# Optimization experiments

Measured on AMD Instinct MI355X. Metric: run time of the kernel, lower is better.

## Reference

```python
import jax, jax.numpy as jnp
import numpy as np

D_MODEL = 1024
N_HEADS = 16
MIXTURE_FACTOR = 4
LATENT = D_MODEL // MIXTURE_FACTOR  # 256
D_K = D_MODEL // N_HEADS            # 64
B, L = 2, 2048


def setup_inputs() -> dict:
    key = jax.random.key(0)
    ks = jax.random.split(key, 13)
    s_in = 1.0 / np.sqrt(D_MODEL)
    s_lat = 1.0 / np.sqrt(LATENT)
    return {
        "queries": jax.random.normal(ks[0], (B, L, 1, D_MODEL), jnp.float32),
        "keys": jax.random.normal(ks[1], (B, L, 1, D_MODEL), jnp.float32),
        "values": jax.random.normal(ks[2], (B, L, 1, D_MODEL), jnp.float32),
        "Wq": jax.random.normal(ks[3], (D_MODEL, D_MODEL), jnp.float32) * s_in,
        "bq": jnp.zeros((D_MODEL,), jnp.float32),
        "Wd": jax.random.normal(ks[4], (D_MODEL, LATENT), jnp.float32) * s_in,
        "bd": jnp.zeros((LATENT,), jnp.float32),
        "Wk": jax.random.normal(ks[5], (LATENT, D_MODEL), jnp.float32) * s_lat,
        "bk": jnp.zeros((D_MODEL,), jnp.float32),
        "Wv": jax.random.normal(ks[6], (LATENT, D_MODEL), jnp.float32) * s_lat,
        "bv": jnp.zeros((D_MODEL,), jnp.float32),
        "Wo": jax.random.normal(ks[7], (D_MODEL, D_MODEL), jnp.float32) * s_in,
        "bo": jnp.zeros((D_MODEL,), jnp.float32),
    }


def reference(queries, keys, values, Wq, bq, Wd, bd, Wk, bk, Wv, bv, Wo, bo):
    b, l, h_in, e = queries.shape  # h_in == 1, e == d_model
    s = keys.shape[1]
    scale = D_K ** -0.5

    q_flat = queries.reshape(b, l, e)
    Q = (q_flat @ Wq + bq).reshape(b, l, N_HEADS, D_K)

    kv_input = keys.reshape(b, s, e)
    latent = kv_input @ Wd + bd                      # [b, s, latent]
    K = (latent @ Wk + bk).reshape(b, s, N_HEADS, D_K)
    V = (latent @ Wv + bv).reshape(b, s, N_HEADS, D_K)

    scores = jnp.einsum('blhe,bshe->bhls', Q, K) * scale  # [b, h, l, s]
    causal = jnp.triu(jnp.ones((l, s), dtype=bool), k=1)
    scores = jnp.where(causal, -jnp.inf, scores)
    A = jax.nn.softmax(scores, axis=-1)

    out = jnp.einsum('bhls,bshd->blhd', A, V).reshape(b, l, N_HEADS * D_K)
    return out @ Wo + bo
```

## Files before the change

### kernel.cpp

```cpp
#include <hip/hip_runtime.h>
#include <stdint.h>


#define DM 1024
#define NH 16
#define DK 64
#define LL 2048

typedef float  f32x4  __attribute__((ext_vector_type(4)));
typedef __bf16 bf16x8 __attribute__((ext_vector_type(8)));
typedef short  s16x8  __attribute__((ext_vector_type(8)));

__device__ __forceinline__ unsigned short f2bf(float f) {
    union { float f; unsigned int u; } v; v.f = f;
    return (unsigned short)((v.u + 0x7fffu + ((v.u >> 16) & 1u)) >> 16);
}
__device__ __forceinline__ unsigned int pack2(float a, float b) {
    return (unsigned int)f2bf(a) | ((unsigned int)f2bf(b) << 16);
}
__device__ __forceinline__ unsigned int packt(float a, float b) {
    union { float f; unsigned int u; } x, y; x.f = a; y.f = b;
    return (x.u >> 16) | (y.u & 0xffff0000u);
}
__device__ __forceinline__ bf16x8 ld8(const unsigned short* p) {
    s16x8 s = *(const s16x8*)p;
    return __builtin_bit_cast(bf16x8, s);
}
__device__ __forceinline__ void gl16(const void* g, void* l) {
    __builtin_amdgcn_global_load_lds((__attribute__((address_space(1))) void*)(g),
                                     (__attribute__((address_space(3))) void*)(l),
                                     16, 0, 0);
}

__global__ __launch_bounds__(256)
void prep_k(const float* __restrict__ Wq, const float* __restrict__ Wd,
            const float* __restrict__ Wk, const float* __restrict__ Wv,
            const float* __restrict__ Wo, const float* __restrict__ queries,
            const float* __restrict__ keys,
            unsigned short* __restrict__ WqT, unsigned short* __restrict__ WdT,
            unsigned short* __restrict__ WkvT, unsigned short* __restrict__ WoT,
            unsigned short* __restrict__ Qb, unsigned short* __restrict__ Kb) {
    int bid = blockIdx.x;
    const int t = threadIdx.x;

    const float* W; unsigned short* WT; int TK, TN;
    if (bid < 1024)      { W = Wq; WT = WqT;  TK = 1024; TN = 1024; }
    else if (bid < 1280) { bid -= 1024; W = Wd; WT = WdT; TK = 1024; TN = 256; }
    else if (bid < 1536) { bid -= 1280; W = Wk; WT = WkvT; TK = 256; TN = 1024; }
    else if (bid < 1792) { bid -= 1536; W = Wv; WT = WkvT + (size_t)1024 * 256; TK = 256; TN = 1024; }
    else if (bid < 2816) { bid -= 1792; W = Wo; WT = WoT;  TK = 1024; TN = 1024; }
    else {
        bid -= 2816;
        const float* src; unsigned short* dst;
        if (bid < 1024) { src = queries; dst = Qb; }
        else            { bid -= 1024; src = keys; dst = Kb; }
        const size_t base = (size_t)bid * 4096;
#pragma unroll
        for (int i = 0; i < 4; ++i) {
            float4 f = *(const float4*)(src + base + (size_t)(i * 256 + t) * 4);
            uint2 u = { pack2(f.x, f.y), pack2(f.z, f.w) };
            *(uint2*)(dst + base + (size_t)(i * 256 + t) * 4) = u;
        }
        return;
    }
    __shared__ float tile[32][33];
    const int tx = t & 31, ty = t >> 5;
    const int bx = bid % (TK / 32), by = bid / (TK / 32);
    const int k0 = bx * 32, n0 = by * 32;
#pragma unroll
    for (int i = 0; i < 4; ++i)
        tile[ty + 8 * i][tx] = W[(size_t)(k0 + ty + 8 * i) * TN + n0 + tx];
    __syncthreads();
#pragma unroll
    for (int i = 0; i < 4; ++i)
        WT[(size_t)(n0 + ty + 8 * i) * TK + k0 + tx] = f2bf(tile[tx][ty + 8 * i]);
}

__device__ __forceinline__ void stage6(const unsigned short* gA, const unsigned short* gB,
                                       int kk, int K,
                                       unsigned short* lA, unsigned short* lB) {
#pragma unroll
    for (int s = 0; s < 4; ++s) gl16(gA + kk + (size_t)s * 8 * K, lA + s * 512);
#pragma unroll
    for (int s = 0; s < 2; ++s) gl16(gB + kk + (size_t)s * 8 * K, lB + s * 512);
}

__device__ __forceinline__ void mfma16(const unsigned short* As, const unsigned short* Bs,
                                       const int aoff[4][2], const int boff[2][2],
                                       f32x4 acc[4][2]) {
#pragma unroll
    for (int ks = 0; ks < 2; ++ks) {
        bf16x8 a[4], b[2];
#pragma unroll
        for (int i = 0; i < 4; ++i) a[i] = ld8(As + aoff[i][ks]);
#pragma unroll
        for (int j = 0; j < 2; ++j) b[j] = ld8(Bs + boff[j][ks]);
#pragma unroll
        for (int i = 0; i < 4; ++i)
#pragma unroll
            for (int j = 0; j < 2; ++j)
                acc[i][j] = __builtin_amdgcn_mfma_f32_16x16x32_bf16(a[i], b[j], acc[i][j], 0, 0, 0);
    }
}

template<int MODE>
__global__ __launch_bounds__(256)
void gemm_k(const unsigned short* __restrict__ Ap, const unsigned short* __restrict__ Bt,
            const float* __restrict__ bias, void* __restrict__ Cp,
            const unsigned short* __restrict__ Ap2, const unsigned short* __restrict__ Bt2,
            const float* __restrict__ bias2, void* __restrict__ Cp2,
            int K) {
    __shared__ unsigned short Sh0[12288];
    __shared__ unsigned short Sh1[12288];

    int bid = blockIdx.x;
    const unsigned short* A;
    const unsigned short* B;
    const float* bs;
    bool second = false;
    int m0, n0;
    if (MODE == 0 && bid >= 512) {
        bid -= 512; A = Ap2; B = Bt2; bs = bias2; second = true;
        const int xcd = bid & 7, s = bid >> 3;
        n0 = (s & 3) * 64; m0 = (xcd * 4 + (s >> 2)) * 128;
    } else {
        A = Ap; B = Bt; bs = bias;
        const int xcd = bid & 7, s = bid >> 3;
        if (MODE == 2) { n0 = (s & 31) * 64; m0 = (xcd * 4 + (s >> 5)) * 128; }
        else           { n0 = (s & 15) * 64; m0 = (xcd * 4 + (s >> 4)) * 128; }
    }

    const int t = threadIdx.x, lane = t & 63, wv = t >> 6;
    const int quad = lane >> 4, l15 = lane & 15;

    const int lr8 = lane >> 3;
    const int g8 = (lane & 7) ^ (lr8 & 7);
    const unsigned short* gA = A + (size_t)(m0 + wv * 32 + lr8) * K + g8 * 8;
    const unsigned short* gB = B + (size_t)(n0 + wv * 16 + lr8) * K + g8 * 8;
    unsigned short* lA0 = Sh0 + wv * 2048;
    unsigned short* lB0 = Sh0 + 8192 + wv * 1024;
    unsigned short* lA1 = Sh1 + wv * 2048;
    unsigned short* lB1 = Sh1 + 8192 + wv * 1024;

    int aoff[4][2], boff[2][2];
#pragma unroll
    for (int i = 0; i < 4; ++i) {
        const int ra = (wv >> 1) * 64 + i * 16 + l15;
#pragma unroll
        for (int ks = 0; ks < 2; ++ks)
            aoff[i][ks] = ra * 64 + (((ks * 4 + quad) ^ (ra & 7)) << 3);
    }
#pragma unroll
    for (int j = 0; j < 2; ++j) {
        const int rb = (wv & 1) * 32 + j * 16 + l15;
#pragma unroll
        for (int ks = 0; ks < 2; ++ks)
            boff[j][ks] = rb * 64 + (((ks * 4 + quad) ^ (rb & 7)) << 3);
    }

    f32x4 acc[4][2] = {};
    const int niter = K >> 6;

    stage6(gA, gB, 0, K, lA0, lB0);
    __syncthreads();
    for (int it = 0; it < niter; it += 2) {
        const int kk = it << 6;
        if (it + 1 < niter) stage6(gA, gB, kk + 64, K, lA1, lB1);
        mfma16(Sh0, Sh0 + 8192, aoff, boff, acc);
        __syncthreads();
        if (it + 1 < niter) {
            if (it + 2 < niter) stage6(gA, gB, kk + 128, K, lA0, lB0);
            mfma16(Sh1, Sh1 + 8192, aoff, boff, acc);
            __syncthreads();
        }
    }

    const bool isV = (MODE == 2) && (n0 >= 1024);
    if (!isV) {
#pragma unroll
        for (int j = 0; j < 2; ++j) {
            const int col = n0 + (wv & 1) * 32 + j * 16 + l15;
            const float bvv = bs[col];
#pragma unroll
            for (int i = 0; i < 4; ++i) {
                const int rowb = m0 + (wv >> 1) * 64 + i * 16 + quad * 4;
#pragma unroll
                for (int r = 0; r < 4; ++r) {
                    const float v = acc[i][j][r] + bvv;
                    const int row = rowb + r;
                    if (MODE == 1)
                        ((float*)Cp)[(size_t)row * 1024 + col] = v;
                    else if (second)
                        ((unsigned short*)Cp2)[(size_t)row * 256 + col] = f2bf(v);
                    else
                        ((unsigned short*)Cp)[(size_t)row * 1024 + col] = f2bf(v);
                }
            }
        }
    } else {
        unsigned short* Ld = Sh0;
#pragma unroll
        for (int j = 0; j < 2; ++j) {
            const int dloc = (wv & 1) * 32 + j * 16 + l15;
            const float bvv = bias2[(n0 - 1024) + dloc];
#pragma unroll
            for (int i = 0; i < 4; ++i) {
                const int tokb = (wv >> 1) * 64 + i * 16 + quad * 4;
#pragma unroll
                for (int r = 0; r < 4; ++r)
                    Ld[dloc * 136 + tokb + r] = f2bf(acc[i][j][r] + bvv);
            }
        }
        __syncthreads();
        const int dloc = t >> 2;
        const int tk0 = (t & 3) * 32;
        const int bb = m0 >> 11;
        unsigned short* dst = (unsigned short*)Cp2 +
            ((size_t)bb * 1024 + (n0 - 1024) + dloc) * LL + (m0 & (LL - 1)) + tk0;
        const unsigned short* srcp = Ld + dloc * 136 + tk0;
#pragma unroll
        for (int c = 0; c < 4; ++c)
            *(uint4*)(dst + c * 8) = *(const uint4*)(srcp + c * 8);
    }
}

__global__ __launch_bounds__(512, 4)
void attn8_k(const unsigned short* __restrict__ Qp,
             const unsigned short* __restrict__ Kp,
             const unsigned short* __restrict__ VpT,
             unsigned short* __restrict__ Op) {
    __shared__ unsigned short Ks[2][2][4096];
    __shared__ unsigned short Vs[2][4096];
    __shared__ unsigned short Ps[8][1152];
    float* CB = (float*)&Ks[0][0][0];

    const int t = threadIdx.x, lane = t & 63, wv = t >> 6;
    const int grp = wv >> 2, w4 = wv & 3;
    const int quad = lane >> 4, l15 = lane & 15;

    const int bid = blockIdx.x;
    const int xcd = bid & 7, s = bid >> 3;
    const int pair = s & 15;
    const int combo = xcd * 4 + (s >> 4);
    const int h = combo & 15, b = combo >> 4;

    const int srow = w4 * 16 + (lane >> 3);
    const int g8 = (lane & 7) ^ ((lane >> 3) & 7);
    const int sw = l15 & 7;
    unsigned short* PsW = Ps[wv];

    const unsigned short* Kbase = Kp + (size_t)(b * LL + srow) * DM + h * DK + g8 * 8;
    const unsigned short* Vbase = VpT + ((size_t)(b * NH + h) * DK + srow) * LL + g8 * 8;
    unsigned short* lV = &Vs[grp][w4 * 1024];

    for (int tsel = 0; tsel < 2; ++tsel) {
        const int tile = tsel ? (31 - pair) : pair;
        const int q0 = tile * 64;
        const int rowq = q0 + w4 * 16 + l15;

        if (tsel) __syncthreads();

        const unsigned short* qp = Qp + (size_t)(b * LL + rowq) * DM + h * DK;
        const bf16x8 aq0 = ld8(qp + quad * 8);
        const bf16x8 aq1 = ld8(qp + 32 + quad * 8);

        f32x4 acc[4] = {};
        float lsum = 0.f;

        if (grp <= tile) {
            const unsigned short* kg = Kbase + (size_t)(grp * 64) * DM;
            unsigned short* lK = &Ks[grp][0][w4 * 1024];
            gl16(kg, lK); gl16(kg + (size_t)8 * DM, lK + 512);
        }

        const int nit = tile / 2 + 1;
        for (int it = 0; it < nit; ++it) {
            const int c = 2 * it + grp;
            const int cur = it & 1;
            const bool active = (c <= tile);
            const int kt = c * 64;

            if (active) {
                const unsigned short* vg = Vbase + kt;
                gl16(vg, lV); gl16(vg + (size_t)8 * LL, lV + 512);
                const int c2 = (c + 2 <= tile) ? (c + 2) : tile;
                const unsigned short* kg = Kbase + (size_t)(c2 * 64) * DM;
                unsigned short* lK = &Ks[grp][cur ^ 1][w4 * 1024];
                gl16(kg, lK); gl16(kg + (size_t)8 * DM, lK + 512);
            }
            asm volatile("s_waitcnt vmcnt(4)" ::: "memory");
            __builtin_amdgcn_s_barrier();
            __builtin_amdgcn_sched_barrier(0);

            if (active) {
                const unsigned short* Kc = Ks[grp][cur];
                const bool diag = (c == tile);
#pragma unroll
                for (int sub = 0; sub < 4; ++sub) {
                    const int base2 = (sub * 16 + l15) * 64;
                    const bf16x8 k0 = ld8(Kc + base2 + ((quad ^ sw) << 3));
                    const bf16x8 k1 = ld8(Kc + base2 + (((4 + quad) ^ sw) << 3));
                    f32x4 ss = {};
                    ss = __builtin_amdgcn_mfma_f32_16x16x32_bf16(k0, aq0, ss, 0, 0, 0);
                    ss = __builtin_amdgcn_mfma_f32_16x16x32_bf16(k1, aq1, ss, 0, 0, 0);
                    float e[4];
                    if (diag) {
                        const int kb4 = kt + sub * 16 + quad * 4;
#pragma unroll
                        for (int r = 0; r < 4; ++r) {
                            const float x = exp2f(fmaf(ss[r], 0.18033688011112042f, -16.0f));
                            e[r] = (kb4 + r > rowq) ? 0.f : x;
                        }
                    } else {
#pragma unroll
                        for (int r = 0; r < 4; ++r)
                            e[r] = exp2f(fmaf(ss[r], 0.18033688011112042f, -16.0f));
                    }
                    lsum += (e[0] + e[1]) + (e[2] + e[3]);
                    uint2 w2;
                    w2.x = packt(e[0], e[1]);
                    w2.y = packt(e[2], e[3]);
                    *(uint2*)(PsW + l15 * 72 + sub * 16 + quad * 4) = w2;
                }
            }
            asm volatile("s_waitcnt vmcnt(2)" ::: "memory");
            __builtin_amdgcn_s_barrier();
            __builtin_amdgcn_sched_barrier(0);

            if (active) {
#pragma unroll
                for (int ks = 0; ks < 2; ++ks) {
                    const bf16x8 ap = ld8(PsW + l15 * 72 + ks * 32 + quad * 8);
#pragma unroll
                    for (int sub = 0; sub < 4; ++sub) {
                        const bf16x8 bv = ld8(&Vs[grp][(sub * 16 + l15) * 64 +
                                                       (((ks * 4 + quad) ^ sw) << 3)]);
                        acc[sub] = __builtin_amdgcn_mfma_f32_16x16x32_bf16(ap, bv, acc[sub], 0, 0, 0);
                    }
                }
            }
            __builtin_amdgcn_s_barrier();
            __builtin_amdgcn_sched_barrier(0);
        }

        __syncthreads();
        const int base = (w4 * 64 + lane) * 20;
        if (grp == 1) {
#pragma unroll
            for (int sub = 0; sub < 4; ++sub)
#pragma unroll
                for (int r = 0; r < 4; ++r) CB[base + sub * 4 + r] = acc[sub][r];
            CB[base + 16] = lsum;
        }
        __syncthreads();
        if (grp == 0) {
#pragma unroll
            for (int sub = 0; sub < 4; ++sub)
#pragma unroll
                for (int r = 0; r < 4; ++r) acc[sub][r] += CB[base + sub * 4 + r];
            lsum += CB[base + 16];
            lsum += __shfl_xor(lsum, 16, 64);
            lsum += __shfl_xor(lsum, 32, 64);
            const float inv = __builtin_amdgcn_rcpf(lsum);
            float invr[4];
#pragma unroll
            for (int r = 0; r < 4; ++r) invr[r] = __shfl(inv, quad * 4 + r, 64);
#pragma unroll
            for (int sub = 0; sub < 4; ++sub)
#pragma unroll
                for (int r = 0; r < 4; ++r)
                    Op[(size_t)(b * LL + q0 + w4 * 16 + quad * 4 + r) * DM + h * DK + sub * 16 + l15] =
                        f2bf(acc[sub][r] * invr[r]);
        }
    }
}

extern "C" void kernel_launch(void* const* d_in, const int* in_sizes, int n_in,
                              void* d_out, int out_size, void* d_ws, size_t ws_size,
                              hipStream_t stream) {
    const float* queries = (const float*)d_in[0];
    const float* keys    = (const float*)d_in[1];
    const float* Wq = (const float*)d_in[3];  const float* bq = (const float*)d_in[4];
    const float* Wd = (const float*)d_in[5];  const float* bd = (const float*)d_in[6];
    const float* Wk = (const float*)d_in[7];  const float* bk = (const float*)d_in[8];
    const float* Wv = (const float*)d_in[9];  const float* bv = (const float*)d_in[10];
    const float* Wo = (const float*)d_in[11]; const float* bo = (const float*)d_in[12];

    char* ws = (char*)d_ws;
    const size_t MB = 1048576;
    unsigned short* Qp   = (unsigned short*)(ws);
    unsigned short* Kb   = (unsigned short*)(ws + 8 * MB);
    unsigned short* Kp   = (unsigned short*)(ws + 8 * MB);
    unsigned short* Qb   = (unsigned short*)(ws + 16 * MB);
    unsigned short* VpT  = (unsigned short*)(ws + 16 * MB);
    unsigned short* WqT  = (unsigned short*)(ws + 24 * MB);
    unsigned short* Lat  = (unsigned short*)(ws + 26 * MB);
    unsigned short* WdT  = (unsigned short*)(ws + 28 * MB);
    unsigned short* WkvT = (unsigned short*)(ws + 28 * MB + 524288);
    unsigned short* Attn = (unsigned short*)(ws + 24 * MB);
    unsigned short* WoT  = (unsigned short*)(ws + 32 * MB);

    prep_k<<<4864, 256, 0, stream>>>(Wq, Wd, Wk, Wv, Wo, queries, keys,
                                     WqT, WdT, WkvT, WoT, Qb, Kb);
    gemm_k<0><<<640, 256, 0, stream>>>(Qb, WqT, bq, Qp, Kb, WdT, bd, Lat, 1024);
    gemm_k<2><<<1024, 256, 0, stream>>>(Lat, WkvT, bk, Kp, nullptr, nullptr, bv, VpT, 256);
    attn8_k<<<512, 512, 0, stream>>>(Qp, Kp, VpT, Attn);
    gemm_k<1><<<512, 256, 0, stream>>>(Attn, WoT, bo, d_out, nullptr, nullptr, nullptr, nullptr, 1024);
}
```

Measured before the change: 202.2 us.

## Share K/V tile loads between paired query tiles in one causal attention sweep

The attention kernel now processes its two query tiles (pair and 31-pair) in a single pass over key blocks instead of two sequential passes. Each K/V tile loaded into LDS is used for both tiles when the smaller tile is still active, which removes the duplicate global loads for the short tile. It also wraps the MFMA sections in s_setprio raises. The cost is doubled accumulator registers and a longer serial inner phase per iteration, where the A-tile QK and PV run back to back through the same P buffer, which could hurt occupancy or latency hiding.

```diff
diff --git a/kernel.cpp b/kernel.cpp
--- a/kernel.cpp
+++ b/kernel.cpp
@@ -224,8 +224,57 @@
     }
 }
 
+__device__ __forceinline__ void qk_sm(const unsigned short* Kc,
+        const bf16x8 aq0, const bf16x8 aq1, int rowq, int kt, bool diag,
+        int l15, int quad, int sw, unsigned short* PsW, float& lsum) {
+#pragma unroll
+    for (int sub = 0; sub < 4; ++sub) {
+        const int base2 = (sub * 16 + l15) * 64;
+        const bf16x8 k0 = ld8(Kc + base2 + ((quad ^ sw) << 3));
+        const bf16x8 k1 = ld8(Kc + base2 + (((4 + quad) ^ sw) << 3));
+        f32x4 ss = {};
+        __builtin_amdgcn_s_setprio(1);
+        ss = __builtin_amdgcn_mfma_f32_16x16x32_bf16(k0, aq0, ss, 0, 0, 0);
+        ss = __builtin_amdgcn_mfma_f32_16x16x32_bf16(k1, aq1, ss, 0, 0, 0);
+        __builtin_amdgcn_s_setprio(0);
+        float e[4];
+        if (diag) {
+            const int kb4 = kt + sub * 16 + quad * 4;
+#pragma unroll
+            for (int r = 0; r < 4; ++r) {
+                const float x = exp2f(fmaf(ss[r], 0.18033688011112042f, -16.0f));
+                e[r] = (kb4 + r > rowq) ? 0.f : x;
+            }
+        } else {
+#pragma unroll
+            for (int r = 0; r < 4; ++r)
+                e[r] = exp2f(fmaf(ss[r], 0.18033688011112042f, -16.0f));
+        }
+        lsum += (e[0] + e[1]) + (e[2] + e[3]);
+        uint2 w2;
+        w2.x = packt(e[0], e[1]);
+        w2.y = packt(e[2], e[3]);
+        *(uint2*)(PsW + l15 * 72 + sub * 16 + quad * 4) = w2;
+    }
+}
+
+__device__ __forceinline__ void pv_acc(const unsigned short* PsW, const unsigned short* Vg,
+        int l15, int quad, int sw, f32x4 acc[4]) {
+#pragma unroll
+    for (int ks = 0; ks < 2; ++ks) {
+        const bf16x8 ap = ld8(PsW + l15 * 72 + ks * 32 + quad * 8);
+        __builtin_amdgcn_s_setprio(1);
+#pragma unroll
+        for (int sub = 0; sub < 4; ++sub) {
+            const bf16x8 bv = ld8(Vg + (sub * 16 + l15) * 64 + (((ks * 4 + quad) ^ sw) << 3));
+            acc[sub] = __builtin_amdgcn_mfma_f32_16x16x32_bf16(ap, bv, acc[sub], 0, 0, 0);
+        }
+        __builtin_amdgcn_s_setprio(0);
+    }
+}
+
 __global__ __launch_bounds__(512, 4)
-void attn8_k(const unsigned short* __restrict__ Qp,
+void attn9_k(const unsigned short* __restrict__ Qp,
              const unsigned short* __restrict__ Kp,
              const unsigned short* __restrict__ VpT,
              unsigned short* __restrict__ Op) {
@@ -244,6 +293,8 @@
     const int combo = xcd * 4 + (s >> 4);
     const int h = combo & 15, b = combo >> 4;
 
+    const int tA = pair, tB = 31 - pair;
+
     const int srow = w4 * 16 + (lane >> 3);
     const int g8 = (lane & 7) ^ ((lane >> 3) & 7);
     const int sw = l15 & 7;
@@ -253,125 +304,117 @@
     const unsigned short* Vbase = VpT + ((size_t)(b * NH + h) * DK + srow) * LL + g8 * 8;
     unsigned short* lV = &Vs[grp][w4 * 1024];
 
-    for (int tsel = 0; tsel < 2; ++tsel) {
-        const int tile = tsel ? (31 - pair) : pair;
-        const int q0 = tile * 64;
-        const int rowq = q0 + w4 * 16 + l15;
-
-        if (tsel) __syncthreads();
-
-        const unsigned short* qp = Qp + (size_t)(b * LL + rowq) * DM + h * DK;
-        const bf16x8 aq0 = ld8(qp + quad * 8);
-        const bf16x8 aq1 = ld8(qp + 32 + quad * 8);
-
-        f32x4 acc[4] = {};
-        float lsum = 0.f;
-
-        if (grp <= tile) {
-            const unsigned short* kg = Kbase + (size_t)(grp * 64) * DM;
-            unsigned short* lK = &Ks[grp][0][w4 * 1024];
+    const int rowqA = tA * 64 + w4 * 16 + l15;
+    const int rowqB = tB * 64 + w4 * 16 + l15;
+    const unsigned short* qpA = Qp + (size_t)(b * LL + rowqA) * DM + h * DK;
+    const unsigned short* qpB = Qp + (size_t)(b * LL + rowqB) * DM + h * DK;
+    const bf16x8 aqA0 = ld8(qpA + quad * 8), aqA1 = ld8(qpA + 32 + quad * 8);
+    const bf16x8 aqB0 = ld8(qpB + quad * 8), aqB1 = ld8(qpB + 32 + quad * 8);
+
+    f32x4 accA[4] = {}, accB[4] = {};
+    float lsumA = 0.f, lsumB = 0.f;
+
+    {
+        const unsigned short* kg = Kbase + (size_t)(grp * 64) * DM;
+        unsigned short* lK = &Ks[grp][0][w4 * 1024];
+        gl16(kg, lK); gl16(kg + (size_t)8 * DM, lK + 512);
+    }
+    const int lastc = tB - ((tB ^ grp) & 1);
+
+    const int nit = tB / 2 + 1;
+    for (int it = 0; it < nit; ++it) {
+        const int c = 2 * it + grp;
+        const int cur = it & 1;
+        const bool activeB = (c <= tB);
+        const bool activeA = (c <= tA);
+        const int kt = c * 64;
+
+        if (activeB) {
+            const unsigned short* vg = Vbase + kt;
+            gl16(vg, lV); gl16(vg + (size_t)8 * LL, lV + 512);
+            const int c2 = (c + 2 <= lastc) ? (c + 2) : lastc;
+            const unsigned short* kg = Kbase + (size_t)(c2 * 64) * DM;
+            unsigned short* lK = &Ks[grp][cur ^ 1][w4 * 1024];
             gl16(kg, lK); gl16(kg + (size_t)8 * DM, lK + 512);
         }
-
-        const int nit = tile / 2 + 1;
-        for (int it = 0; it < nit; ++it) {
-            const int c = 2 * it + grp;
-            const int cur = it & 1;
-            const bool active = (c <= tile);
-            const int kt = c * 64;
-
-            if (active) {
-                const unsigned short* vg = Vbase + kt;
-                gl16(vg, lV); gl16(vg + (size_t)8 * LL, lV + 512);
-                const int c2 = (c + 2 <= tile) ? (c + 2) : tile;
-                const unsigned short* kg = Kbase + (size_t)(c2 * 64) * DM;
-                unsigned short* lK = &Ks[grp][cur ^ 1][w4 * 1024];
-                gl16(kg, lK); gl16(kg + (size_t)8 * DM, lK + 512);
-            }
-            asm volatile("s_waitcnt vmcnt(4)" ::: "memory");
-            __builtin_amdgcn_s_barrier();
-            __builtin_amdgcn_sched_barrier(0);
-
-            if (active) {
-                const unsigned short* Kc = Ks[grp][cur];
-                const bool diag = (c == tile);
-#pragma unroll
-                for (int sub = 0; sub < 4; ++sub) {
-                    const int base2 = (sub * 16 + l15) * 64;
-                    const bf16x8 k0 = ld8(Kc + base2 + ((quad ^ sw) << 3));
-                    const bf16x8 k1 = ld8(Kc + base2 + (((4 + quad) ^ sw) << 3));
-                    f32x4 ss = {};
-                    ss = __builtin_amdgcn_mfma_f32_16x16x32_bf16(k0, aq0, ss, 0, 0, 0);
-                    ss = __builtin_amdgcn_mfma_f32_16x16x32_bf16(k1, aq1, ss, 0, 0, 0);
-                    float e[4];
-                    if (diag) {
-                        const int kb4 = kt + sub * 16 + quad * 4;
-#pragma unroll
-                        for (int r = 0; r < 4; ++r) {
-                            const float x = exp2f(fmaf(ss[r], 0.18033688011112042f, -16.0f));
-                            e[r] = (kb4 + r > rowq) ? 0.f : x;
-                        }
-                    } else {
-#pragma unroll
-                        for (int r = 0; r < 4; ++r)
-                            e[r] = exp2f(fmaf(ss[r], 0.18033688011112042f, -16.0f));
-                    }
-                    lsum += (e[0] + e[1]) + (e[2] + e[3]);
-                    uint2 w2;
-                    w2.x = packt(e[0], e[1]);
-                    w2.y = packt(e[2], e[3]);
-                    *(uint2*)(PsW + l15 * 72 + sub * 16 + quad * 4) = w2;
-                }
-            }
-            asm volatile("s_waitcnt vmcnt(2)" ::: "memory");
-            __builtin_amdgcn_s_barrier();
-            __builtin_amdgcn_sched_barrier(0);
-
-            if (active) {
-#pragma unroll
-                for (int ks = 0; ks < 2; ++ks) {
-                    const bf16x8 ap = ld8(PsW + l15 * 72 + ks * 32 + quad * 8);
-#pragma unroll
-                    for (int sub = 0; sub < 4; ++sub) {
-                        const bf16x8 bv = ld8(&Vs[grp][(sub * 16 + l15) * 64 +
-                                                       (((ks * 4 + quad) ^ sw) << 3)]);
-                        acc[sub] = __builtin_amdgcn_mfma_f32_16x16x32_bf16(ap, bv, acc[sub], 0, 0, 0);
-                    }
-                }
-            }
-            __builtin_amdgcn_s_barrier();
-            __builtin_amdgcn_sched_barrier(0);
-        }
-
-        __syncthreads();
-        const int base = (w4 * 64 + lane) * 20;
-        if (grp == 1) {
-#pragma unroll
-            for (int sub = 0; sub < 4; ++sub)
-#pragma unroll
-                for (int r = 0; r < 4; ++r) CB[base + sub * 4 + r] = acc[sub][r];
-            CB[base + 16] = lsum;
-        }
-        __syncthreads();
-        if (grp == 0) {
-#pragma unroll
-            for (int sub = 0; sub < 4; ++sub)
-#pragma unroll
-                for (int r = 0; r < 4; ++r) acc[sub][r] += CB[base + sub * 4 + r];
-            lsum += CB[base + 16];
-            lsum += __shfl_xor(lsum, 16, 64);
-            lsum += __shfl_xor(lsum, 32, 64);
-            const float inv = __builtin_amdgcn_rcpf(lsum);
-            float invr[4];
-#pragma unroll
-            for (int r = 0; r < 4; ++r) invr[r] = __shfl(inv, quad * 4 + r, 64);
-#pragma unroll
-            for (int sub = 0; sub < 4; ++sub)
-#pragma unroll
-                for (int r = 0; r < 4; ++r)
-                    Op[(size_t)(b * LL + q0 + w4 * 16 + quad * 4 + r) * DM + h * DK + sub * 16 + l15] =
-                        f2bf(acc[sub][r] * invr[r]);
-        }
+        asm volatile("s_waitcnt vmcnt(4)" ::: "memory");
+        __builtin_amdgcn_s_barrier();
+        __builtin_amdgcn_sched_barrier(0);
+
+        const unsigned short* Kc = Ks[grp][cur];
+        if (activeB)
+            qk_sm(Kc, aqB0, aqB1, rowqB, kt, c == tB, l15, quad, sw, PsW, lsumB);
+
+        asm volatile("s_waitcnt vmcnt(2)" ::: "memory");
+        __builtin_amdgcn_s_barrier();
+        __builtin_amdgcn_sched_barrier(0);
+
+        if (activeB)
+            pv_acc(PsW, &Vs[grp][0], l15, quad, sw, accB);
+        if (activeA) {
+            qk_sm(Kc, aqA0, aqA1, rowqA, kt, c == tA, l15, quad, sw, PsW, lsumA);
+            pv_acc(PsW, &Vs[grp][0], l15, quad, sw, accA);
+        }
+        __builtin_amdgcn_s_barrier();
+        __builtin_amdgcn_sched_barrier(0);
+    }
+
+    __syncthreads();
+    const int base = (w4 * 64 + lane) * 20;
+    if (grp == 1) {
+#pragma unroll
+        for (int sub = 0; sub < 4; ++sub)
+#pragma unroll
+            for (int r = 0; r < 4; ++r) CB[base + sub * 4 + r] = accA[sub][r];
+        CB[base + 16] = lsumA;
+    }
+    __syncthreads();
+    if (grp == 0) {
+#pragma unroll
+        for (int sub = 0; sub < 4; ++sub)
+#pragma unroll
+            for (int r = 0; r < 4; ++r) accA[sub][r] += CB[base + sub * 4 + r];
+        lsumA += CB[base + 16];
+        lsumA += __shfl_xor(lsumA, 16, 64);
+        lsumA += __shfl_xor(lsumA, 32, 64);
+        const float inv = __builtin_amdgcn_rcpf(lsumA);
+        float invr[4];
+#pragma unroll
+        for (int r = 0; r < 4; ++r) invr[r] = __shfl(inv, quad * 4 + r, 64);
+#pragma unroll
+        for (int sub = 0; sub < 4; ++sub)
+#pragma unroll
+            for (int r = 0; r < 4; ++r)
+                Op[(size_t)(b * LL + tA * 64 + w4 * 16 + quad * 4 + r) * DM + h * DK + sub * 16 + l15] =
+                    f2bf(accA[sub][r] * invr[r]);
+    }
+    __syncthreads();
+    if (grp == 1) {
+#pragma unroll
+        for (int sub = 0; sub < 4; ++sub)
+#pragma unroll
+            for (int r = 0; r < 4; ++r) CB[base + sub * 4 + r] = accB[sub][r];
+        CB[base + 16] = lsumB;
+    }
+    __syncthreads();
+    if (grp == 0) {
+#pragma unroll
+        for (int sub = 0; sub < 4; ++sub)
+#pragma unroll
+            for (int r = 0; r < 4; ++r) accB[sub][r] += CB[base + sub * 4 + r];
+        lsumB += CB[base + 16];
+        lsumB += __shfl_xor(lsumB, 16, 64);
+        lsumB += __shfl_xor(lsumB, 32, 64);
+        const float inv = __builtin_amdgcn_rcpf(lsumB);
+        float invr[4];
+#pragma unroll
+        for (int r = 0; r < 4; ++r) invr[r] = __shfl(inv, quad * 4 + r, 64);
+#pragma unroll
+        for (int sub = 0; sub < 4; ++sub)
+#pragma unroll
+            for (int r = 0; r < 4; ++r)
+                Op[(size_t)(b * LL + tB * 64 + w4 * 16 + quad * 4 + r) * DM + h * DK + sub * 16 + l15] =
+                    f2bf(accB[sub][r] * invr[r]);
     }
 }
 
@@ -404,6 +447,6 @@
                                      WqT, WdT, WkvT, WoT, Qb, Kb);
     gemm_k<0><<<640, 256, 0, stream>>>(Qb, WqT, bq, Qp, Kb, WdT, bd, Lat, 1024);
     gemm_k<2><<<1024, 256, 0, stream>>>(Lat, WkvT, bk, Kp, nullptr, nullptr, bv, VpT, 256);
-    attn8_k<<<512, 512, 0, stream>>>(Qp, Kp, VpT, Attn);
+    attn9_k<<<512, 512, 0, stream>>>(Qp, Kp, VpT, Attn);
     gemm_k<1><<<512, 256, 0, stream>>>(Attn, WoT, bo, d_out, nullptr, nullptr, nullptr, nullptr, 1024);
 }
```

Result: slower. 207.0 us (+2.3%).

## Replace split-KV paired-tile attention with one-tile-per-block 256-thread kernel

Applied to the files above, without the earlier changes.

The attention kernel previously had each 512-thread block process two query tiles (pair and 31-pair), splitting the KV range between two wave groups and merging their partial results through LDS. The new kernel launches 1024 blocks of 256 threads, each handling one query tile with a single-group double-buffered KV loop and no cross-group reduction. Tiles are ordered long-first within each XCD slot, relying on the hardware scheduler for causal load balancing. s_setprio is also added around the MFMA sections. This removes the merge and the idle-group iterations, but a single wave group per tile now serialises the KV loop and gives less intra-block parallelism per tile.

```diff
diff --git a/kernel.cpp b/kernel.cpp
--- a/kernel.cpp
+++ b/kernel.cpp
@@ -224,155 +224,135 @@
     }
 }
 
-__global__ __launch_bounds__(512, 4)
-void attn8_k(const unsigned short* __restrict__ Qp,
-             const unsigned short* __restrict__ Kp,
-             const unsigned short* __restrict__ VpT,
-             unsigned short* __restrict__ Op) {
-    __shared__ unsigned short Ks[2][2][4096];
-    __shared__ unsigned short Vs[2][4096];
-    __shared__ unsigned short Ps[8][1152];
-    float* CB = (float*)&Ks[0][0][0];
+__device__ __forceinline__ void qk_sm(const unsigned short* Kc,
+        const bf16x8 aq0, const bf16x8 aq1, int rowq, int kt, bool diag,
+        int l15, int quad, int sw, unsigned short* PsW, float& lsum) {
+#pragma unroll
+    for (int sub = 0; sub < 4; ++sub) {
+        const int base2 = (sub * 16 + l15) * 64;
+        const bf16x8 k0 = ld8(Kc + base2 + ((quad ^ sw) << 3));
+        const bf16x8 k1 = ld8(Kc + base2 + (((4 + quad) ^ sw) << 3));
+        f32x4 ss = {};
+        __builtin_amdgcn_s_setprio(1);
+        ss = __builtin_amdgcn_mfma_f32_16x16x32_bf16(k0, aq0, ss, 0, 0, 0);
+        ss = __builtin_amdgcn_mfma_f32_16x16x32_bf16(k1, aq1, ss, 0, 0, 0);
+        __builtin_amdgcn_s_setprio(0);
+        float e[4];
+        if (diag) {
+            const int kb4 = kt + sub * 16 + quad * 4;
+#pragma unroll
+            for (int r = 0; r < 4; ++r) {
+                const float x = exp2f(fmaf(ss[r], 0.18033688011112042f, -16.0f));
+                e[r] = (kb4 + r > rowq) ? 0.f : x;
+            }
+        } else {
+#pragma unroll
+            for (int r = 0; r < 4; ++r)
+                e[r] = exp2f(fmaf(ss[r], 0.18033688011112042f, -16.0f));
+        }
+        lsum += (e[0] + e[1]) + (e[2] + e[3]);
+        uint2 w2;
+        w2.x = packt(e[0], e[1]);
+        w2.y = packt(e[2], e[3]);
+        *(uint2*)(PsW + l15 * 72 + sub * 16 + quad * 4) = w2;
+    }
+}
+
+__device__ __forceinline__ void pv_acc(const unsigned short* PsW, const unsigned short* Vg,
+        int l15, int quad, int sw, f32x4 acc[4]) {
+#pragma unroll
+    for (int ks = 0; ks < 2; ++ks) {
+        const bf16x8 ap = ld8(PsW + l15 * 72 + ks * 32 + quad * 8);
+        __builtin_amdgcn_s_setprio(1);
+#pragma unroll
+        for (int sub = 0; sub < 4; ++sub) {
+            const bf16x8 bv = ld8(Vg + (sub * 16 + l15) * 64 + (((ks * 4 + quad) ^ sw) << 3));
+            acc[sub] = __builtin_amdgcn_mfma_f32_16x16x32_bf16(ap, bv, acc[sub], 0, 0, 0);
+        }
+        __builtin_amdgcn_s_setprio(0);
+    }
+}
+
+__global__ __launch_bounds__(256, 4)
+void attn10_k(const unsigned short* __restrict__ Qp,
+              const unsigned short* __restrict__ Kp,
+              const unsigned short* __restrict__ VpT,
+              unsigned short* __restrict__ Op) {
+    __shared__ unsigned short Ks[2][4096];
+    __shared__ unsigned short Vs[4096];
+    __shared__ unsigned short Ps[4][1152];
 
     const int t = threadIdx.x, lane = t & 63, wv = t >> 6;
-    const int grp = wv >> 2, w4 = wv & 3;
     const int quad = lane >> 4, l15 = lane & 15;
 
     const int bid = blockIdx.x;
     const int xcd = bid & 7, s = bid >> 3;
-    const int pair = s & 15;
-    const int combo = xcd * 4 + (s >> 4);
+    const int cu = s & 31, slot = s >> 5;
+    const int combo = xcd * 4 + slot;
+    const int tile = (slot & 1) ? cu : (31 - cu);
     const int h = combo & 15, b = combo >> 4;
-
-    const int srow = w4 * 16 + (lane >> 3);
+    const int q0 = tile * 64;
+
+    const int srow = wv * 16 + (lane >> 3);
     const int g8 = (lane & 7) ^ ((lane >> 3) & 7);
     const int sw = l15 & 7;
     unsigned short* PsW = Ps[wv];
 
     const unsigned short* Kbase = Kp + (size_t)(b * LL + srow) * DM + h * DK + g8 * 8;
     const unsigned short* Vbase = VpT + ((size_t)(b * NH + h) * DK + srow) * LL + g8 * 8;
-    unsigned short* lV = &Vs[grp][w4 * 1024];
-
-    for (int tsel = 0; tsel < 2; ++tsel) {
-        const int tile = tsel ? (31 - pair) : pair;
-        const int q0 = tile * 64;
-        const int rowq = q0 + w4 * 16 + l15;
-
-        if (tsel) __syncthreads();
-
-        const unsigned short* qp = Qp + (size_t)(b * LL + rowq) * DM + h * DK;
-        const bf16x8 aq0 = ld8(qp + quad * 8);
-        const bf16x8 aq1 = ld8(qp + 32 + quad * 8);
-
-        f32x4 acc[4] = {};
-        float lsum = 0.f;
-
-        if (grp <= tile) {
-            const unsigned short* kg = Kbase + (size_t)(grp * 64) * DM;
-            unsigned short* lK = &Ks[grp][0][w4 * 1024];
-            gl16(kg, lK); gl16(kg + (size_t)8 * DM, lK + 512);
-        }
-
-        const int nit = tile / 2 + 1;
-        for (int it = 0; it < nit; ++it) {
-            const int c = 2 * it + grp;
-            const int cur = it & 1;
-            const bool active = (c <= tile);
-            const int kt = c * 64;
-
-            if (active) {
-                const unsigned short* vg = Vbase + kt;
-                gl16(vg, lV); gl16(vg + (size_t)8 * LL, lV + 512);
-                const int c2 = (c + 2 <= tile) ? (c + 2) : tile;
-                const unsigned short* kg = Kbase + (size_t)(c2 * 64) * DM;
-                unsigned short* lK = &Ks[grp][cur ^ 1][w4 * 1024];
-                gl16(kg, lK); gl16(kg + (size_t)8 * DM, lK + 512);
-            }
-            asm volatile("s_waitcnt vmcnt(4)" ::: "memory");
-            __builtin_amdgcn_s_barrier();
-            __builtin_amdgcn_sched_barrier(0);
-
-            if (active) {
-                const unsigned short* Kc = Ks[grp][cur];
-                const bool diag = (c == tile);
-#pragma unroll
-                for (int sub = 0; sub < 4; ++sub) {
-                    const int base2 = (sub * 16 + l15) * 64;
-                    const bf16x8 k0 = ld8(Kc + base2 + ((quad ^ sw) << 3));
-                    const bf16x8 k1 = ld8(Kc + base2 + (((4 + quad) ^ sw) << 3));
-                    f32x4 ss = {};
-                    ss = __builtin_amdgcn_mfma_f32_16x16x32_bf16(k0, aq0, ss, 0, 0, 0);
-                    ss = __builtin_amdgcn_mfma_f32_16x16x32_bf16(k1, aq1, ss, 0, 0, 0);
-                    float e[4];
-                    if (diag) {
-                        const int kb4 = kt + sub * 16 + quad * 4;
-#pragma unroll
-                        for (int r = 0; r < 4; ++r) {
-                            const float x = exp2f(fmaf(ss[r], 0.18033688011112042f, -16.0f));
-                            e[r] = (kb4 + r > rowq) ? 0.f : x;
-                        }
-                    } else {
-#pragma unroll
-                        for (int r = 0; r < 4; ++r)
-                            e[r] = exp2f(fmaf(ss[r], 0.18033688011112042f, -16.0f));
-                    }
-                    lsum += (e[0] + e[1]) + (e[2] + e[3]);
-                    uint2 w2;
-                    w2.x = packt(e[0], e[1]);
-                    w2.y = packt(e[2], e[3]);
-                    *(uint2*)(PsW + l15 * 72 + sub * 16 + quad * 4) = w2;
-                }
-            }
-            asm volatile("s_waitcnt vmcnt(2)" ::: "memory");
-            __builtin_amdgcn_s_barrier();
-            __builtin_amdgcn_sched_barrier(0);
-
-            if (active) {
-#pragma unroll
-                for (int ks = 0; ks < 2; ++ks) {
-                    const bf16x8 ap = ld8(PsW + l15 * 72 + ks * 32 + quad * 8);
-#pragma unroll
-                    for (int sub = 0; sub < 4; ++sub) {
-                        const bf16x8 bv = ld8(&Vs[grp][(sub * 16 + l15) * 64 +
-                                                       (((ks * 4 + quad) ^ sw) << 3)]);
-                        acc[sub] = __builtin_amdgcn_mfma_f32_16x16x32_bf16(ap, bv, acc[sub], 0, 0, 0);
-                    }
-                }
-            }
-            __builtin_amdgcn_s_barrier();
-            __builtin_amdgcn_sched_barrier(0);
-        }
-
-        __syncthreads();
-        const int base = (w4 * 64 + lane) * 20;
-        if (grp == 1) {
-#pragma unroll
-            for (int sub = 0; sub < 4; ++sub)
-#pragma unroll
-                for (int r = 0; r < 4; ++r) CB[base + sub * 4 + r] = acc[sub][r];
-            CB[base + 16] = lsum;
-        }
-        __syncthreads();
-        if (grp == 0) {
-#pragma unroll
-            for (int sub = 0; sub < 4; ++sub)
-#pragma unroll
-                for (int r = 0; r < 4; ++r) acc[sub][r] += CB[base + sub * 4 + r];
-            lsum += CB[base + 16];
-            lsum += __shfl_xor(lsum, 16, 64);
-            lsum += __shfl_xor(lsum, 32, 64);
-            const float inv = __builtin_amdgcn_rcpf(lsum);
-            float invr[4];
-#pragma unroll
-            for (int r = 0; r < 4; ++r) invr[r] = __shfl(inv, quad * 4 + r, 64);
-#pragma unroll
-            for (int sub = 0; sub < 4; ++sub)
-#pragma unroll
-                for (int r = 0; r < 4; ++r)
-                    Op[(size_t)(b * LL + q0 + w4 * 16 + quad * 4 + r) * DM + h * DK + sub * 16 + l15] =
-                        f2bf(acc[sub][r] * invr[r]);
-        }
-    }
+    unsigned short* lV = Vs + wv * 1024;
+
+    const int rowq = q0 + wv * 16 + l15;
+    const unsigned short* qp = Qp + (size_t)(b * LL + rowq) * DM + h * DK;
+    const bf16x8 aq0 = ld8(qp + quad * 8);
+    const bf16x8 aq1 = ld8(qp + 32 + quad * 8);
+
+    f32x4 acc[4] = {};
+    float lsum = 0.f;
+
+    gl16(Kbase, Ks[0] + wv * 1024);
+    gl16(Kbase + (size_t)8 * DM, Ks[0] + wv * 1024 + 512);
+
+    for (int c = 0; c <= tile; ++c) {
+        const int cur = c & 1;
+        const int kt = c * 64;
+
+        const unsigned short* vg = Vbase + kt;
+        gl16(vg, lV); gl16(vg + (size_t)8 * LL, lV + 512);
+        const int c2 = (c + 1 <= tile) ? (c + 1) : tile;
+        const unsigned short* kg = Kbase + (size_t)(c2 * 64) * DM;
+        unsigned short* lK = Ks[cur ^ 1] + wv * 1024;
+        gl16(kg, lK); gl16(kg + (size_t)8 * DM, lK + 512);
+
+        asm volatile("s_waitcnt vmcnt(4)" ::: "memory");
+        __builtin_amdgcn_s_barrier();
+        __builtin_amdgcn_sched_barrier(0);
+
+        qk_sm(Ks[cur], aq0, aq1, rowq, kt, c == tile, l15, quad, sw, PsW, lsum);
+
+        asm volatile("s_waitcnt vmcnt(2)" ::: "memory");
+        __builtin_amdgcn_s_barrier();
+        __builtin_amdgcn_sched_barrier(0);
+
+        pv_acc(PsW, Vs, l15, quad, sw, acc);
+
+        __builtin_amdgcn_s_barrier();
+        __builtin_amdgcn_sched_barrier(0);
+    }
+    asm volatile("s_waitcnt vmcnt(0)" ::: "memory");
+
+    lsum += __shfl_xor(lsum, 16, 64);
+    lsum += __shfl_xor(lsum, 32, 64);
+    const float inv = __builtin_amdgcn_rcpf(lsum);
+    float invr[4];
+#pragma unroll
+    for (int r = 0; r < 4; ++r) invr[r] = __shfl(inv, quad * 4 + r, 64);
+#pragma unroll
+    for (int sub = 0; sub < 4; ++sub)
+#pragma unroll
+        for (int r = 0; r < 4; ++r)
+            Op[(size_t)(b * LL + q0 + wv * 16 + quad * 4 + r) * DM + h * DK + sub * 16 + l15] =
+                f2bf(acc[sub][r] * invr[r]);
 }
 
 extern "C" void kernel_launch(void* const* d_in, const int* in_sizes, int n_in,
@@ -404,6 +384,6 @@
                                      WqT, WdT, WkvT, WoT, Qb, Kb);
     gemm_k<0><<<640, 256, 0, stream>>>(Qb, WqT, bq, Qp, Kb, WdT, bd, Lat, 1024);
     gemm_k<2><<<1024, 256, 0, stream>>>(Lat, WkvT, bk, Kp, nullptr, nullptr, bv, VpT, 256);
-    attn8_k<<<512, 512, 0, stream>>>(Qp, Kp, VpT, Attn);
+    attn10_k<<<1024, 256, 0, stream>>>(Qp, Kp, VpT, Attn);
     gemm_k<1><<<512, 256, 0, stream>>>(Attn, WoT, bo, d_out, nullptr, nullptr, nullptr, nullptr, 1024);
 }
```

After: 202.2 us. About the same (-0.0%).
